# Performance work log

Hardware: AMD Instinct MI355X
Metric: run time of the kernel (lower is better)

Reference implementation:

```python
import jax, jax.numpy as jnp
import numpy as np

POOL_SIZE = 7
NUM_ROIS = 1024
H, W, C = 256, 256, 512


def setup_inputs() -> dict:
    key = jax.random.key(0)
    k_img, k_xy, k_wh = jax.random.split(key, 3)
    img = jax.random.normal(k_img, (1, H, W, C), dtype=jnp.float32)
    # Valid ROIs: top-left in [0, 192), size in [8, 64), clipped to image bounds.
    xy = jax.random.randint(k_xy, (1, NUM_ROIS, 2), 0, 192)          # (x1, y1)
    wh = jax.random.randint(k_wh, (1, NUM_ROIS, 2), 8, 64)           # (w, h)
    x1y1 = xy
    x2y2 = jnp.minimum(xy + wh, jnp.array([W, H]))
    rois = jnp.concatenate([x1y1, x2y2], axis=-1).astype(jnp.int32)  # [1, R, 4] = (x1, y1, x2, y2)
    return {"img": img, "rois": rois}


def _roi_resize(feat, roi, P):
    """Bilinear-resize crop feat[y1:y2, x1:x2, :] to (P, P) — TF1 legacy mapping.
    feat: [H, W, C] float, roi: [4] int32 (x1, y1, x2, y2). Returns [P, P, C]."""
    x1, y1, x2, y2 = roi[0], roi[1], roi[2], roi[3]
    h = (y2 - y1).astype(jnp.float32)
    w = (x2 - x1).astype(jnp.float32)
    # src coordinate (crop-relative) = out_idx * (in_size / out_size)
    ys = jnp.arange(P, dtype=jnp.float32) * (h / P)   # [P]
    xs = jnp.arange(P, dtype=jnp.float32) * (w / P)   # [P]
    y0 = jnp.floor(ys).astype(jnp.int32)
    x0 = jnp.floor(xs).astype(jnp.int32)
    y1i = jnp.minimum(y0 + 1, jnp.maximum(y2 - y1 - 1, 0))
    x1i = jnp.minimum(x0 + 1, jnp.maximum(x2 - x1 - 1, 0))
    wy = (ys - y0.astype(jnp.float32))[:, None, None]  # [P,1,1]
    wx = (xs - x0.astype(jnp.float32))[None, :, None]  # [1,P,1]
    r0, r1 = y1 + y0, y1 + y1i                         # absolute rows
    c0, c1 = x1 + x0, x1 + x1i                         # absolute cols
    v00 = feat[r0[:, None], c0[None, :], :]            # [P,P,C]
    v01 = feat[r0[:, None], c1[None, :], :]
    v10 = feat[r1[:, None], c0[None, :], :]
    v11 = feat[r1[:, None], c1[None, :], :]
    return (v00 * (1.0 - wy) * (1.0 - wx) + v01 * (1.0 - wy) * wx
            + v10 * wy * (1.0 - wx) + v11 * wy * wx)


def reference(img, rois):
    feat = img[0]                                       # [H, W, C]
    pooled = jax.vmap(_roi_resize, in_axes=(None, 0, None))(feat, rois[0], POOL_SIZE)
    return pooled[None]                                 # [1, num_rois, P, P, C]
```

## Files before the change

### kernel.cpp

```cpp
#include <hip/hip_runtime.h>

#define POOL 7
#define IMG_W 256
#define IMG_C 512
#define NUM_ROIS 1024

typedef float f4 __attribute__((ext_vector_type(4)));

__global__ __launch_bounds__(1024) void sort_rois_kernel(
    const int* __restrict__ rois, int* __restrict__ order)
{
    __shared__ int hist[64];
    __shared__ int base[64];
    const int tid = threadIdx.x;

    if (tid < 64) hist[tid] = 0;
    __syncthreads();

    const int x1 = rois[4 * tid + 0];
    const int y1 = rois[4 * tid + 1];
    const int key = ((y1 >> 5) << 3) | (x1 >> 5);
    const int rank = atomicAdd(&hist[key], 1);
    __syncthreads();

    if (tid == 0) {
        int run = 0;
#pragma unroll
        for (int k = 0; k < 64; ++k) { base[k] = run; run += hist[k]; }
    }
    __syncthreads();

    order[base[key] + rank] = tid;
}

__global__ __launch_bounds__(128) void roi_pool_kernel(
    const float* __restrict__ img,
    const int*   __restrict__ rois,
    const int*   __restrict__ order,
    float*       __restrict__ out)
{
    const int bid  = blockIdx.x;
    const int xcd  = bid & 7;
    const int slot = bid >> 3;
    const int sloc = slot / POOL;
    const int py   = slot - sloc * POOL;
    const int sidx = xcd * (NUM_ROIS / 8) + sloc;
    const int roi  = order[sidx];

    const int4 rb = ((const int4*)rois)[roi];
    const int x1 = __builtin_amdgcn_readfirstlane(rb.x);
    const int y1 = __builtin_amdgcn_readfirstlane(rb.y);
    const int x2 = __builtin_amdgcn_readfirstlane(rb.z);
    const int y2 = __builtin_amdgcn_readfirstlane(rb.w);

    const float h = (float)(y2 - y1);
    const float w = (float)(x2 - x1);
    const float sy = h / (float)POOL;
    const float sx = w / (float)POOL;

    const float ys = (float)py * sy;
    const int   y0 = (int)floorf(ys);
    const int   y1i = min(y0 + 1, max(y2 - y1 - 1, 0));
    const float wy = ys - (float)y0;

    const size_t rowstride = (size_t)IMG_W * IMG_C;
    const float* row0 = img + (size_t)(y1 + y0)  * rowstride;
    const float* row1 = img + (size_t)(y1 + y1i) * rowstride;

    const int t = threadIdx.x;
    const int cmax = max(x2 - x1 - 1, 0);

    f4* obase = (f4*)out + ((size_t)roi * (POOL * POOL) + (size_t)py * POOL) * (IMG_C / 4) + t;

#pragma unroll
    for (int px = 0; px < POOL; ++px) {
        const float xs = (float)px * sx;
        const int   x0 = (int)floorf(xs);
        const int   x1i = min(x0 + 1, cmax);
        const float wx = xs - (float)x0;
        const int c0 = x1 + x0, c1 = x1 + x1i;

        const f4 v00 = ((const f4*)(row0 + (size_t)c0 * IMG_C))[t];
        const f4 v01 = ((const f4*)(row0 + (size_t)c1 * IMG_C))[t];
        const f4 v10 = ((const f4*)(row1 + (size_t)c0 * IMG_C))[t];
        const f4 v11 = ((const f4*)(row1 + (size_t)c1 * IMG_C))[t];

        const float w00 = (1.0f - wy) * (1.0f - wx);
        const float w01 = (1.0f - wy) * wx;
        const float w10 = wy * (1.0f - wx);
        const float w11 = wy * wx;

        f4 o = v00 * w00 + v01 * w01 + v10 * w10 + v11 * w11;
        __builtin_nontemporal_store(o, obase + px * (IMG_C / 4));
    }
}

extern "C" void kernel_launch(void* const* d_in, const int* in_sizes, int n_in,
                              void* d_out, int out_size, void* d_ws, size_t ws_size,
                              hipStream_t stream) {
    const float* img  = (const float*)d_in[0];
    const int*   rois = (const int*)d_in[1];
    float* out = (float*)d_out;
    int* order = (int*)d_ws;

    sort_rois_kernel<<<1, 1024, 0, stream>>>(rois, order);
    roi_pool_kernel<<<NUM_ROIS * POOL, 128, 0, stream>>>(img, rois, order, out);
}
```

Measured before the change: 234.9 us.

## Split channels into 64-wide chunks across XCDs and map px to thread groups

Each block now handles one ROI row for one 64-channel chunk, with the chunk index taken from the low three bits of the block id. That places one channel slice per XCD instead of one group of spatially sorted ROIs per XCD. Inside a block, 7 groups of 16 threads each compute one output pixel, so 16 of the 128 threads do nothing. The grid is eight times larger. The aim is for each XCD's L2 to cache only its channel slice of the image, at the cost of per-block overhead, shorter 256-byte contiguous accesses, and wasted lanes.

After: 238.2 us. About the same (+1.4%).

```diff
diff --git a/kernel.cpp b/kernel.cpp
--- a/kernel.cpp
+++ b/kernel.cpp
@@ -4,6 +4,8 @@
 #define IMG_W 256
 #define IMG_C 512
 #define NUM_ROIS 1024
+#define CCHUNK 64
+#define NCHUNK (IMG_C / CCHUNK)
 
 typedef float f4 __attribute__((ext_vector_type(4)));
 
@@ -39,13 +41,12 @@
     const int*   __restrict__ order,
     float*       __restrict__ out)
 {
-    const int bid  = blockIdx.x;
-    const int xcd  = bid & 7;
-    const int slot = bid >> 3;
-    const int sloc = slot / POOL;
-    const int py   = slot - sloc * POOL;
-    const int sidx = xcd * (NUM_ROIS / 8) + sloc;
-    const int roi  = order[sidx];
+    const int bid   = blockIdx.x;
+    const int chunk = bid & 7;
+    const int slot  = bid >> 3;
+    const int sidx  = slot / POOL;
+    const int py    = slot - sidx * POOL;
+    const int roi   = order[sidx];
 
     const int4 rb = ((const int4*)rois)[roi];
     const int x1 = __builtin_amdgcn_readfirstlane(rb.x);
@@ -64,26 +65,26 @@
     const float wy = ys - (float)y0;
 
     const size_t rowstride = (size_t)IMG_W * IMG_C;
-    const float* row0 = img + (size_t)(y1 + y0)  * rowstride;
-    const float* row1 = img + (size_t)(y1 + y1i) * rowstride;
+    const size_t choff = (size_t)chunk * CCHUNK;
+    const float* row0 = img + (size_t)(y1 + y0)  * rowstride + choff;
+    const float* row1 = img + (size_t)(y1 + y1i) * rowstride + choff;
 
-    const int t = threadIdx.x;
-    const int cmax = max(x2 - x1 - 1, 0);
+    const int t  = threadIdx.x;
+    const int s  = t >> 4;
+    const int cg = t & 15;
 
-    f4* obase = (f4*)out + ((size_t)roi * (POOL * POOL) + (size_t)py * POOL) * (IMG_C / 4) + t;
-
-#pragma unroll
-    for (int px = 0; px < POOL; ++px) {
-        const float xs = (float)px * sx;
+    if (s < POOL) {
+        const int cmax = max(x2 - x1 - 1, 0);
+        const float xs = (float)s * sx;
         const int   x0 = (int)floorf(xs);
         const int   x1i = min(x0 + 1, cmax);
         const float wx = xs - (float)x0;
         const int c0 = x1 + x0, c1 = x1 + x1i;
 
-        const f4 v00 = ((const f4*)(row0 + (size_t)c0 * IMG_C))[t];
-        const f4 v01 = ((const f4*)(row0 + (size_t)c1 * IMG_C))[t];
-        const f4 v10 = ((const f4*)(row1 + (size_t)c0 * IMG_C))[t];
-        const f4 v11 = ((const f4*)(row1 + (size_t)c1 * IMG_C))[t];
+        const f4 v00 = ((const f4*)(row0 + (size_t)c0 * IMG_C))[cg];
+        const f4 v01 = ((const f4*)(row0 + (size_t)c1 * IMG_C))[cg];
+        const f4 v10 = ((const f4*)(row1 + (size_t)c0 * IMG_C))[cg];
+        const f4 v11 = ((const f4*)(row1 + (size_t)c1 * IMG_C))[cg];
 
         const float w00 = (1.0f - wy) * (1.0f - wx);
         const float w01 = (1.0f - wy) * wx;
@@ -91,7 +92,9 @@
         const float w11 = wy * wx;
 
         f4 o = v00 * w00 + v01 * w01 + v10 * w10 + v11 * w11;
-        __builtin_nontemporal_store(o, obase + px * (IMG_C / 4));
+
+        f4* po = (f4*)(out + (((size_t)roi * (POOL * POOL) + (size_t)py * POOL + s) * IMG_C) + choff);
+        __builtin_nontemporal_store(o, po + cg);
     }
 }
 
@@ -104,5 +107,5 @@
     int* order = (int*)d_ws;
 
     sort_rois_kernel<<<1, 1024, 0, stream>>>(rois, order);
-    roi_pool_kernel<<<NUM_ROIS * POOL, 128, 0, stream>>>(img, rois, order, out);
+    roi_pool_kernel<<<NUM_ROIS * POOL * NCHUNK, 128, 0, stream>>>(img, rois, order, out);
 }
```
